# Kernel optimization log

Hardware: AMD Instinct MI355X
Metric: run time of the kernel (lower is better)

The kernel has to match this reference:

```python
import jax, jax.numpy as jnp
import numpy as np

N_NODES = 50000
N_EDGES = 1600000
F_GO, F_RE, F_ME = 512, 256, 256
E_DIM, N_HEADS, H_DIM, O_DIM = 256, 4, 256, 128


def setup_inputs() -> dict:
    key = jax.random.key(0)
    ks = jax.random.split(key, 20)
    s = lambda k, shp, sc: jax.random.normal(k, shp, dtype=jnp.float32) * sc
    inp = {
        "x": jax.random.normal(ks[0], (N_NODES, F_GO + F_RE + F_ME + 1), dtype=jnp.float32),
        "edge_index": jax.random.randint(ks[1], (2, N_EDGES), 0, N_NODES, dtype=jnp.int32),
        # modality projections (stored as [in, out] so we do x @ W)
        "w_go": s(ks[2], (F_GO, E_DIM), 0.04), "b_go": jnp.zeros((E_DIM,), jnp.float32),
        "w_re": s(ks[3], (F_RE, E_DIM), 0.06), "b_re": jnp.zeros((E_DIM,), jnp.float32),
        "w_me": s(ks[4], (F_ME, E_DIM), 0.06), "b_me": jnp.zeros((E_DIM,), jnp.float32),
        "w_gw": s(ks[5], (1, E_DIM), 0.5),    "b_gw": jnp.zeros((E_DIM,), jnp.float32),
        # MultiheadAttention params (torch layout: in_proj_w [3E, E], out_proj_w [E, E])
        "in_proj_w": s(ks[6], (3 * E_DIM, E_DIM), 0.06),
        "in_proj_b": jnp.zeros((3 * E_DIM,), jnp.float32),
        "out_proj_w": s(ks[7], (E_DIM, E_DIM), 0.06),
        "out_proj_b": jnp.zeros((E_DIM,), jnp.float32),
        # GCN layers (stored as [in, out])
        "w1": s(ks[8], (E_DIM, H_DIM), 0.06), "b1": jnp.zeros((H_DIM,), jnp.float32),
        "w2": s(ks[9], (H_DIM, O_DIM), 0.06), "b2": jnp.zeros((O_DIM,), jnp.float32),
    }
    return inp


def _forward(x, edge_index, w_go, b_go, w_re, b_re, w_me, b_me, w_gw, b_gw,
             in_proj_w, in_proj_b, out_proj_w, out_proj_b, w1, b1, w2, b2):
    N = x.shape[0]
    relu = jax.nn.relu
    go = x[:, :F_GO]
    re_ = x[:, F_GO:F_GO + F_RE]
    me = x[:, F_GO + F_RE:F_GO + F_RE + F_ME]
    gw = x[:, -1:]  # gwas = last column
    # [N, 4, E]: four projected modalities stacked as a tiny sequence
    p = jnp.stack([relu(go @ w_go + b_go), relu(re_ @ w_re + b_re),
                   relu(me @ w_me + b_me), relu(gw @ w_gw + b_gw)], axis=1)
    # Multihead self-attention over the 4 modality tokens
    wq, wk, wv = jnp.split(in_proj_w, 3, axis=0)
    bq, bk, bv = jnp.split(in_proj_b, 3, axis=0)
    dh = E_DIM // N_HEADS
    q = (p @ wq.T + bq).reshape(N, 4, N_HEADS, dh)
    k = (p @ wk.T + bk).reshape(N, 4, N_HEADS, dh)
    v = (p @ wv.T + bv).reshape(N, 4, N_HEADS, dh)
    scores = jnp.einsum('nqhd,nkhd->nhqk', q, k) / jnp.sqrt(jnp.float32(dh))
    attn = jax.nn.softmax(scores, axis=-1)
    o = jnp.einsum('nhqk,nkhd->nqhd', attn, v).reshape(N, 4, E_DIM)
    o = o @ out_proj_w.T + out_proj_b
    fused = o.mean(axis=1)  # [N, E]
    # GCN normalization with self-loops (shared by both layers)
    loops = jnp.arange(N, dtype=edge_index.dtype)
    src = jnp.concatenate([edge_index[0], loops])
    dst = jnp.concatenate([edge_index[1], loops])
    deg = jax.ops.segment_sum(jnp.ones_like(src, dtype=fused.dtype), dst, num_segments=N)
    dinv = jnp.where(deg > 0, jax.lax.rsqrt(deg), 0.0)
    norm = dinv[src] * dinv[dst]  # [E+N]

    def gcn(h, W, b):
        hw = h @ W  # transform then scatter-aggregate
        msg = norm[:, None] * hw[src]
        return jax.ops.segment_sum(msg, dst, num_segments=N) + b

    h1 = relu(gcn(fused, w1, b1))
    # dropout p=0.3 skipped (eval mode)
    return gcn(h1, w2, b2)


def reference(x, edge_index, w_go, b_go, w_re, b_re, w_me, b_me, w_gw, b_gw,
              in_proj_w, in_proj_b, out_proj_w, out_proj_b, w1, b1, w2, b2):
    return _forward(x, edge_index, w_go, b_go, w_re, b_re, w_me, b_me, w_gw, b_gw,
                    in_proj_w, in_proj_b, out_proj_w, out_proj_b, w1, b1, w2, b2)
```

## Files before the change

kernel.cpp:

```cpp
#include <hip/hip_runtime.h>
#include <cstdint>
#include <cstddef>

#define NN 50000
#define NE 1600000
#define XD 1025

typedef unsigned short ushortt;
typedef __attribute__((ext_vector_type(8))) short short8;
typedef __attribute__((ext_vector_type(4))) float f32x4;

__device__ __forceinline__ float relu_f(float v) { return v > 0.f ? v : 0.f; }
__device__ __forceinline__ float b2f(ushortt u) { return __uint_as_float(((unsigned)u) << 16); }
__device__ __forceinline__ float blo(unsigned u) { return __uint_as_float(u << 16); }
__device__ __forceinline__ float bhi(unsigned u) { return __uint_as_float(u & 0xffff0000u); }
__device__ __forceinline__ ushortt bf16rn(float f) {
    unsigned u = __float_as_uint(f);
    return (ushortt)((u + 0x7fffu + ((u >> 16) & 1u)) >> 16);
}
__device__ __forceinline__ void load_lds16(const void* g, void* l) {
    __builtin_amdgcn_global_load_lds(
        (const __attribute__((address_space(1))) void*)g,
        (__attribute__((address_space(3))) void*)l, 16, 0, 0);
}

template <int ACT>
__global__ __launch_bounds__(256) void gemm_mfma(
    const ushortt* __restrict__ A, int lda,
    const ushortt* __restrict__ Bt,
    ushortt* __restrict__ C, int ldc,
    const float* __restrict__ bias,
    int M, int K)
{
    __shared__ ushortt As[128 * 32];
    __shared__ ushortt Bs[128 * 32];
    const int tid = threadIdx.x;
    const int w = tid >> 6, l = tid & 63;
    const int wr = w >> 1, wc = w & 1;
    const int brow = blockIdx.y << 7;
    const int bcol = blockIdx.x << 7;

    f32x4 acc[4][4] = {};

    const int rA0 = wr * 64 + (l & 15);
    const int rB0 = wc * 64 + (l & 15);
    const int kslot = l >> 4;

    for (int k0 = 0; k0 < K; k0 += 32) {
#pragma unroll
        for (int c = 0; c < 2; ++c) {
            int rl = c * 64 + w * 16 + (l >> 2);
            int csel = (l & 3) ^ (rl & 3);
            int gr = brow + rl; if (gr >= M) gr = M - 1;
            load_lds16(A + (size_t)gr * lda + k0 + csel * 8, &As[(c * 64 + w * 16) * 32]);
        }
#pragma unroll
        for (int c = 0; c < 2; ++c) {
            int rl = c * 64 + w * 16 + (l >> 2);
            int csel = (l & 3) ^ (rl & 3);
            load_lds16(Bt + (size_t)(bcol + rl) * K + k0 + csel * 8, &Bs[(c * 64 + w * 16) * 32]);
        }
        __syncthreads();

        short8 af[4], bf[4];
#pragma unroll
        for (int mi = 0; mi < 4; ++mi) {
            int row = rA0 + mi * 16;
            af[mi] = *(const short8*)&As[row * 32 + ((kslot ^ (row & 3)) << 3)];
        }
#pragma unroll
        for (int ni = 0; ni < 4; ++ni) {
            int row = rB0 + ni * 16;
            bf[ni] = *(const short8*)&Bs[row * 32 + ((kslot ^ (row & 3)) << 3)];
        }
#pragma unroll
        for (int mi = 0; mi < 4; ++mi)
#pragma unroll
            for (int ni = 0; ni < 4; ++ni)
                acc[mi][ni] = __builtin_amdgcn_mfma_f32_16x16x32_bf16(af[mi], bf[ni], acc[mi][ni], 0, 0, 0);
        __syncthreads();
    }

    const int cb = bcol + wc * 64 + (l & 15);
    const int rb = brow + wr * 64 + ((l >> 4) << 2);
#pragma unroll
    for (int mi = 0; mi < 4; ++mi) {
#pragma unroll
        for (int ni = 0; ni < 4; ++ni) {
            int col = cb + ni * 16;
            float bv = bias ? bias[col] : 0.f;
#pragma unroll
            for (int r = 0; r < 4; ++r) {
                int row = rb + mi * 16 + r;
                if (row < M) {
                    float v = acc[mi][ni][r] + bv;
                    if (ACT == 1) v = relu_f(v);
                    C[(size_t)row * ldc + col] = bf16rn(v);
                }
            }
        }
    }
}

__global__ __launch_bounds__(256) void gemm_branches(
    const ushortt* __restrict__ ago, const ushortt* __restrict__ are, const ushortt* __restrict__ ame,
    const ushortt* __restrict__ wgo, const ushortt* __restrict__ wre, const ushortt* __restrict__ wme,
    const float* __restrict__ b_go, const float* __restrict__ b_re, const float* __restrict__ b_me,
    ushortt* __restrict__ p)
{
    const ushortt* A; const ushortt* Bt; const float* bias; int K, lda, coff;
    if (blockIdx.z == 0)      { A = ago; Bt = wgo; bias = b_go; K = 512; lda = 512; coff = 0; }
    else if (blockIdx.z == 1) { A = are; Bt = wre; bias = b_re; K = 256; lda = 256; coff = 256; }
    else                      { A = ame; Bt = wme; bias = b_me; K = 256; lda = 256; coff = 512; }

    __shared__ ushortt As[128 * 32];
    __shared__ ushortt Bs[128 * 32];
    const int tid = threadIdx.x;
    const int w = tid >> 6, l = tid & 63;
    const int wr = w >> 1, wc = w & 1;
    const int brow = blockIdx.y << 7;
    const int bcol = blockIdx.x << 7;

    f32x4 acc[4][4] = {};

    const int rA0 = wr * 64 + (l & 15);
    const int rB0 = wc * 64 + (l & 15);
    const int kslot = l >> 4;

    for (int k0 = 0; k0 < K; k0 += 32) {
#pragma unroll
        for (int c = 0; c < 2; ++c) {
            int rl = c * 64 + w * 16 + (l >> 2);
            int csel = (l & 3) ^ (rl & 3);
            int gr = brow + rl; if (gr >= NN) gr = NN - 1;
            load_lds16(A + (size_t)gr * lda + k0 + csel * 8, &As[(c * 64 + w * 16) * 32]);
        }
#pragma unroll
        for (int c = 0; c < 2; ++c) {
            int rl = c * 64 + w * 16 + (l >> 2);
            int csel = (l & 3) ^ (rl & 3);
            load_lds16(Bt + (size_t)(bcol + rl) * K + k0 + csel * 8, &Bs[(c * 64 + w * 16) * 32]);
        }
        __syncthreads();

        short8 af[4], bf[4];
#pragma unroll
        for (int mi = 0; mi < 4; ++mi) {
            int row = rA0 + mi * 16;
            af[mi] = *(const short8*)&As[row * 32 + ((kslot ^ (row & 3)) << 3)];
        }
#pragma unroll
        for (int ni = 0; ni < 4; ++ni) {
            int row = rB0 + ni * 16;
            bf[ni] = *(const short8*)&Bs[row * 32 + ((kslot ^ (row & 3)) << 3)];
        }
#pragma unroll
        for (int mi = 0; mi < 4; ++mi)
#pragma unroll
            for (int ni = 0; ni < 4; ++ni)
                acc[mi][ni] = __builtin_amdgcn_mfma_f32_16x16x32_bf16(af[mi], bf[ni], acc[mi][ni], 0, 0, 0);
        __syncthreads();
    }

    const int cb = bcol + wc * 64 + (l & 15);
    const int rb = brow + wr * 64 + ((l >> 4) << 2);
#pragma unroll
    for (int mi = 0; mi < 4; ++mi) {
#pragma unroll
        for (int ni = 0; ni < 4; ++ni) {
            int col = cb + ni * 16;
            float bv = bias[col];
#pragma unroll
            for (int r = 0; r < 4; ++r) {
                int row = rb + mi * 16 + r;
                if (row < NN)
                    p[(size_t)row * 1024 + coff + col] = bf16rn(relu_f(acc[mi][ni][r] + bv));
            }
        }
    }
}

__global__ __launch_bounds__(256) void fused_attn_v7(
    const ushortt* __restrict__ p,
    const ushortt* __restrict__ ipw_opt,
    const float* __restrict__ ipb,
    ushortt* __restrict__ pbar)
{
    __shared__ __align__(16) ushortt p_s[32 * 256];
    __shared__ float asum_s[8][4][4];

    const int tid = threadIdx.x;
    const int w = tid >> 6, l = tid & 63;
    const int nb = blockIdx.x << 3;
    const size_t r0 = (size_t)nb * 4;

    {
        const int slot = l & 31;
#pragma unroll
        for (int c = 0; c < 4; ++c) {
            int row = w * 8 + c * 2 + (l >> 5);
            load_lds16(p + (r0 + row) * 256 + ((slot ^ (row & 7)) << 3),
                       &p_s[(w * 8 + c * 2) * 256]);
        }
    }
    __syncthreads();

    const int nq = w << 6;
    f32x4 aq[2][4] = {}, ak[2][4] = {};
    const int ar0 = l & 15, ar1 = ar0 + 16;
#pragma unroll
    for (int kk = 0; kk < 8; ++kk) {
        const int slot = (kk << 2) + (l >> 4);
        short8 a0 = *(const short8*)&p_s[ar0 * 256 + ((slot ^ (ar0 & 7)) << 3)];
        short8 a1 = *(const short8*)&p_s[ar1 * 256 + ((slot ^ (ar1 & 7)) << 3)];
        short8 bq[4], bk[4];
#pragma unroll
        for (int ni = 0; ni < 4; ++ni) {
            const size_t base = ((((size_t)(w * 8 + kk)) * 4 + ni) * 2) * 512 + (size_t)l * 8;
            bq[ni] = *(const short8*)&ipw_opt[base];
            bk[ni] = *(const short8*)&ipw_opt[base + 512];
        }
#pragma unroll
        for (int ni = 0; ni < 4; ++ni) {
            aq[0][ni] = __builtin_amdgcn_mfma_f32_16x16x32_bf16(a0, bq[ni], aq[0][ni], 0, 0, 0);
            aq[1][ni] = __builtin_amdgcn_mfma_f32_16x16x32_bf16(a1, bq[ni], aq[1][ni], 0, 0, 0);
            ak[0][ni] = __builtin_amdgcn_mfma_f32_16x16x32_bf16(a0, bk[ni], ak[0][ni], 0, 0, 0);
            ak[1][ni] = __builtin_amdgcn_mfma_f32_16x16x32_bf16(a1, bk[ni], ak[1][ni], 0, 0, 0);
        }
    }

    float bqv[4], bkv[4];
#pragma unroll
    for (int ni = 0; ni < 4; ++ni) {
        int col = nq + (ni << 4) + (l & 15);
        bqv[ni] = ipb[col];
        bkv[ni] = ipb[256 + col];
    }
#pragma unroll
    for (int mt = 0; mt < 2; ++mt) {
        float s[4][4] = {};
#pragma unroll
        for (int ni = 0; ni < 4; ++ni) {
            float qv[4], kv[4];
#pragma unroll
            for (int r = 0; r < 4; ++r) {
                qv[r] = aq[mt][ni][r] + bqv[ni];
                kv[r] = ak[mt][ni][r] + bkv[ni];
            }
#pragma unroll
            for (int ti = 0; ti < 4; ++ti)
#pragma unroll
                for (int tj = 0; tj < 4; ++tj)
                    s[ti][tj] = fmaf(qv[ti], kv[tj], s[ti][tj]);
        }
#pragma unroll
        for (int m = 1; m <= 8; m <<= 1)
#pragma unroll
            for (int ti = 0; ti < 4; ++ti)
#pragma unroll
                for (int tj = 0; tj < 4; ++tj)
                    s[ti][tj] += __shfl_xor(s[ti][tj], m);
        float asum[4] = {};
#pragma unroll
        for (int ti = 0; ti < 4; ++ti) {
            float v0 = s[ti][0] * 0.125f, v1 = s[ti][1] * 0.125f;
            float v2 = s[ti][2] * 0.125f, v3 = s[ti][3] * 0.125f;
            float m4 = fmaxf(fmaxf(v0, v1), fmaxf(v2, v3));
            float e0 = __expf(v0 - m4), e1 = __expf(v1 - m4);
            float e2 = __expf(v2 - m4), e3 = __expf(v3 - m4);
            float inv = 1.f / (e0 + e1 + e2 + e3);
            asum[0] = fmaf(e0, inv, asum[0]);
            asum[1] = fmaf(e1, inv, asum[1]);
            asum[2] = fmaf(e2, inv, asum[2]);
            asum[3] = fmaf(e3, inv, asum[3]);
        }
        if ((l & 15) == 0) {
            int node = mt * 4 + (l >> 4);
#pragma unroll
            for (int tj = 0; tj < 4; ++tj)
                asum_s[node][w][tj] = 0.25f * asum[tj];
        }
    }
    __syncthreads();

    {
        const int node = tid >> 5;
        const int c8 = (tid & 31) << 3;
        float f[4][8];
#pragma unroll
        for (int tj = 0; tj < 4; ++tj) {
            int row = node * 4 + tj;
            uint4 u = *(const uint4*)&p_s[row * 256 + (((c8 >> 3) ^ (row & 7)) << 3)];
            f[tj][0] = blo(u.x); f[tj][1] = bhi(u.x); f[tj][2] = blo(u.y); f[tj][3] = bhi(u.y);
            f[tj][4] = blo(u.z); f[tj][5] = bhi(u.z); f[tj][6] = blo(u.w); f[tj][7] = bhi(u.w);
        }
#pragma unroll
        for (int h = 0; h < 4; ++h) {
            float a0 = asum_s[node][h][0], a1 = asum_s[node][h][1];
            float a2 = asum_s[node][h][2], a3 = asum_s[node][h][3];
            ushortt res[8];
#pragma unroll
            for (int i = 0; i < 8; ++i)
                res[i] = bf16rn(a0 * f[0][i] + a1 * f[1][i] + a2 * f[2][i] + a3 * f[3][i]);
            *(uint4*)&pbar[(size_t)(nb + node) * 1024 + h * 256 + c8] = *(uint4*)res;
        }
    }
}

__global__ __launch_bounds__(256) void prep_T(
    const float* __restrict__ opw, const float* __restrict__ w1, float* __restrict__ T)
{
    int d = blockIdx.x, c = threadIdx.x;
    float a = 0.f;
    for (int j = 0; j < 256; ++j)
        a = fmaf(opw[j * 256 + d], w1[j * 256 + c], a);
    T[d * 256 + c] = a;
}

__global__ __launch_bounds__(256) void prep_wbig(
    const float* __restrict__ wv, const float* __restrict__ T, ushortt* __restrict__ wbigT)
{
    int c = blockIdx.x, kk = threadIdx.x;
#pragma unroll
    for (int h = 0; h < 4; ++h) {
        float a = 0.f;
        for (int d = 0; d < 64; ++d)
            a = fmaf(wv[(h * 64 + d) * 256 + kk], T[(h * 64 + d) * 256 + c], a);
        wbigT[(size_t)c * 1024 + h * 256 + kk] = bf16rn(a);
    }
}

__global__ __launch_bounds__(256) void prep_bbig(
    const float* __restrict__ opb, const float* __restrict__ w1,
    const float* __restrict__ ipb, const float* __restrict__ T,
    float* __restrict__ bbig)
{
    int c = threadIdx.x;
    float a = 0.f;
    for (int j = 0; j < 256; ++j) a = fmaf(opb[j], w1[j * 256 + c], a);
    for (int d = 0; d < 256; ++d) a = fmaf(ipb[512 + d], T[d * 256 + c], a);
    bbig[c] = a;
}

__global__ __launch_bounds__(256) void conv_all(
    const float* __restrict__ w_go, const float* __restrict__ w_re,
    const float* __restrict__ w_me, const float* __restrict__ w2,
    const float* __restrict__ ipw,
    ushortt* __restrict__ o_go, ushortt* __restrict__ o_re,
    ushortt* __restrict__ o_me, ushortt* __restrict__ o_w2,
    ushortt* __restrict__ o_ip)
{
    int idx = blockIdx.x * 256 + threadIdx.x;
    if (idx < 131072) {
        int c = idx >> 9, r = idx & 511;
        o_go[idx] = bf16rn(w_go[r * 256 + c]);
    } else if (idx < 196608) {
        int j = idx - 131072; int c = j >> 8, r = j & 255;
        o_re[j] = bf16rn(w_re[r * 256 + c]);
    } else if (idx < 262144) {
        int j = idx - 196608; int c = j >> 8, r = j & 255;
        o_me[j] = bf16rn(w_me[r * 256 + c]);
    } else if (idx < 294912) {
        int j = idx - 262144; int c = j >> 8, r = j & 255;
        o_w2[j] = bf16rn(w2[r * 128 + c]);
    } else if (idx < 425984) {
        int j5 = idx - 294912;
        int j  = j5 & 7;
        int l  = (j5 >> 3) & 63;
        int qk = (j5 >> 9) & 1;
        int ni = (j5 >> 10) & 3;
        int kk = (j5 >> 12) & 7;
        int w  = (j5 >> 15) & 3;
        int row = qk * 256 + w * 64 + ni * 16 + (l & 15);
        int col = kk * 32 + ((l >> 4) << 3) + j;
        o_ip[j5] = bf16rn(ipw[(size_t)row * 256 + col]);
    }
}

__global__ __launch_bounds__(256) void conv_x(
    const float* __restrict__ x, ushortt* __restrict__ ago,
    ushortt* __restrict__ are, ushortt* __restrict__ ame)
{
    long idx = blockIdx.x * 256L + threadIdx.x;
    if (idx >= (long)NN * 128) return;
    int n = (int)(idx >> 7);
    int c8 = ((int)idx & 127) << 3;
    const float* src = x + (size_t)n * XD + c8;
    ushortt* dst;
    if (c8 < 512) dst = ago + (size_t)n * 512 + c8;
    else if (c8 < 768) dst = are + (size_t)n * 256 + (c8 - 512);
    else dst = ame + (size_t)n * 256 + (c8 - 768);
    ushort4 o1, o2;
    o1.x = bf16rn(src[0]); o1.y = bf16rn(src[1]); o1.z = bf16rn(src[2]); o1.w = bf16rn(src[3]);
    o2.x = bf16rn(src[4]); o2.y = bf16rn(src[5]); o2.z = bf16rn(src[6]); o2.w = bf16rn(src[7]);
    *(ushort4*)dst = o1;
    *(ushort4*)(dst + 4) = o2;
}

__global__ __launch_bounds__(256) void gw_kernel(
    const float* __restrict__ x, const float* __restrict__ w_gw,
    const float* __restrict__ b_gw, ushortt* __restrict__ p)
{
    long idx = blockIdx.x * 256L + threadIdx.x;
    if (idx >= (long)NN * 64) return;
    int n = (int)(idx >> 6);
    int c = ((int)idx & 63) << 2;
    float g = x[(size_t)n * XD + 1024];
    float4 w4 = *(const float4*)(w_gw + c);
    float4 b4 = *(const float4*)(b_gw + c);
    ushort4 r;
    r.x = bf16rn(relu_f(fmaf(g, w4.x, b4.x)));
    r.y = bf16rn(relu_f(fmaf(g, w4.y, b4.y)));
    r.z = bf16rn(relu_f(fmaf(g, w4.z, b4.z)));
    r.w = bf16rn(relu_f(fmaf(g, w4.w, b4.w)));
    *(ushort4*)(p + (size_t)n * 1024 + 768 + c) = r;
}

__global__ __launch_bounds__(256) void deg_int_kernel(
    const int* __restrict__ dst, int* __restrict__ deg, int E)
{
    int e = (blockIdx.x * 256 + threadIdx.x) * 4;
    if (e >= E) return;
    int4 d = *(const int4*)(dst + e);
    atomicAdd(&deg[d.x], 1);
    atomicAdd(&deg[d.y], 1);
    atomicAdd(&deg[d.z], 1);
    atomicAdd(&deg[d.w], 1);
}

__global__ __launch_bounds__(256) void dinv_kernel(
    const int* __restrict__ deg, float* __restrict__ dinv, int N)
{
    int n = blockIdx.x * 256 + threadIdx.x;
    if (n < N) dinv[n] = rsqrtf((float)deg[n] + 1.0f);
}

__global__ __launch_bounds__(1024) void scan_blk(
    const int* __restrict__ deg, int* __restrict__ offs, int* __restrict__ btot, int N)
{
    __shared__ int wsum[16];
    const int tid = threadIdx.x;
    const int lane = tid & 63;
    const int w = tid >> 6;
    int i = blockIdx.x * 1024 + tid;
    int v = (i < N) ? deg[i] : 0;
    int x = v;
#pragma unroll
    for (int d = 1; d < 64; d <<= 1) {
        int t = __shfl_up(x, d);
        if (lane >= d) x += t;
    }
    if (lane == 63) wsum[w] = x;
    __syncthreads();
    if (w == 0 && lane < 16) {
        int y = wsum[lane];
#pragma unroll
        for (int d = 1; d < 16; d <<= 1) {
            int t = __shfl_up(y, d);
            if (lane >= d) y += t;
        }
        wsum[lane] = y;
    }
    __syncthreads();
    int waveoff = (w == 0) ? 0 : wsum[w - 1];
    if (i < N) offs[i] = waveoff + x - v;
    if (tid == 0) btot[blockIdx.x] = wsum[15];
}

__global__ __launch_bounds__(64) void scan_tot(int* __restrict__ btot, int nb)
{
    int t = threadIdx.x;
    int v = (t < nb) ? btot[t] : 0;
    int x = v;
#pragma unroll
    for (int d = 1; d < 64; d <<= 1) {
        int tt = __shfl_up(x, d);
        if (t >= d) x += tt;
    }
    if (t < nb) btot[t] = x - v;
    if (t == 63) btot[nb] = x;
}

__global__ __launch_bounds__(256) void scan_add(
    const int* __restrict__ btot, int* __restrict__ offs, int N, int nb)
{
    int i = blockIdx.x * 256 + threadIdx.x;
    if (i < N) offs[i] += btot[i >> 10];
    else if (i == N) offs[N] = btot[nb];
}

__global__ __launch_bounds__(256) void csr_fill(
    const int* __restrict__ ei, const int* __restrict__ offs,
    int* __restrict__ cursor, int2* __restrict__ pk,
    const float* __restrict__ dinv, int E)
{
    for (int e = blockIdx.x * 256 + threadIdx.x; e < E; e += gridDim.x * 256) {
        int s = ei[e];
        int d = ei[NE + e];
        int pos = offs[d] + atomicAdd(&cursor[d], 1);
        pk[pos] = make_int2(s, __float_as_int(dinv[s] * dinv[d]));
    }
}

template <int ACT, int OUTBF>
__global__ __launch_bounds__(256) void gcn_gather256(
    const int* __restrict__ offs, const int2* __restrict__ pk,
    const ushortt* __restrict__ hw,
    const float* __restrict__ dinv, const float* __restrict__ bias,
    void* __restrict__ outb, int N)
{
    __shared__ float part[2][256];
    const int tid = threadIdx.x;
    const int nodei = tid >> 7;
    const int half = (tid >> 6) & 1;
    const int l = tid & 63;
    const int wid = blockIdx.x * 2 + nodei;
    const int col = l * 4;
    const bool active = wid < N;

    int beg = 0, end = 0;
    if (active) { beg = offs[wid]; end = offs[wid + 1]; }
    const int mid = beg + ((end - beg + 1) >> 1);
    int e = half ? mid : beg;
    const int ee = half ? end : mid;

    float acc[4] = {0.f, 0.f, 0.f, 0.f};
    if (active && half == 0) {
        float self = dinv[wid] * dinv[wid];
        ushort4 r = *(const ushort4*)(hw + (size_t)wid * 256 + col);
        acc[0] = self * b2f(r.x); acc[1] = self * b2f(r.y);
        acc[2] = self * b2f(r.z); acc[3] = self * b2f(r.w);
    }

    for (; e + 7 < ee; e += 8) {
        int2 q[8];
#pragma unroll
        for (int j = 0; j < 8; ++j) q[j] = pk[e + j];
        ushort4 r[8];
#pragma unroll
        for (int j = 0; j < 8; ++j) r[j] = *(const ushort4*)(hw + (size_t)q[j].x * 256 + col);
#pragma unroll
        for (int j = 0; j < 8; ++j) {
            float n = __int_as_float(q[j].y);
            acc[0] = fmaf(n, b2f(r[j].x), acc[0]); acc[1] = fmaf(n, b2f(r[j].y), acc[1]);
            acc[2] = fmaf(n, b2f(r[j].z), acc[2]); acc[3] = fmaf(n, b2f(r[j].w), acc[3]);
        }
    }
    for (; e < ee; ++e) {
        int2 p0 = pk[e];
        float n0 = __int_as_float(p0.y);
        ushort4 r0 = *(const ushort4*)(hw + (size_t)p0.x * 256 + col);
        acc[0] = fmaf(n0, b2f(r0.x), acc[0]); acc[1] = fmaf(n0, b2f(r0.y), acc[1]);
        acc[2] = fmaf(n0, b2f(r0.z), acc[2]); acc[3] = fmaf(n0, b2f(r0.w), acc[3]);
    }

    if (half == 1) {
        float4 v; v.x = acc[0]; v.y = acc[1]; v.z = acc[2]; v.w = acc[3];
        *(float4*)&part[nodei][col] = v;
    }
    __syncthreads();
    if (active && half == 0) {
        float4 pv = *(const float4*)&part[nodei][col];
        acc[0] += pv.x; acc[1] += pv.y; acc[2] += pv.z; acc[3] += pv.w;
#pragma unroll
        for (int jj = 0; jj < 4; ++jj) {
            acc[jj] += bias[col + jj];
            if (ACT == 1) acc[jj] = relu_f(acc[jj]);
        }
        if (OUTBF == 1) {
            ushortt* ob = (ushortt*)outb;
            ushort4 r;
            r.x = bf16rn(acc[0]); r.y = bf16rn(acc[1]); r.z = bf16rn(acc[2]); r.w = bf16rn(acc[3]);
            *(ushort4*)(ob + (size_t)wid * 256 + col) = r;
        } else {
            float* ob = (float*)outb;
            float4 r; r.x = acc[0]; r.y = acc[1]; r.z = acc[2]; r.w = acc[3];
            *(float4*)(ob + (size_t)wid * 256 + col) = r;
        }
    }
}

__global__ __launch_bounds__(256) void gcn_gather128(
    const int* __restrict__ offs, const int2* __restrict__ pk,
    const ushortt* __restrict__ hw,
    const float* __restrict__ dinv, const float* __restrict__ bias,
    float* __restrict__ outb, int N)
{
    const int wid = blockIdx.x * 4 + (threadIdx.x >> 6);
    const int lane = threadIdx.x & 63;
    if (wid >= N) return;
    const int g = lane >> 5;
    const int col = (lane & 31) * 4;

    float acc[4] = {0.f, 0.f, 0.f, 0.f};
    if (g == 0) {
        float self = dinv[wid] * dinv[wid];
        ushort4 r = *(const ushort4*)(hw + (size_t)wid * 128 + col);
        acc[0] = self * b2f(r.x); acc[1] = self * b2f(r.y);
        acc[2] = self * b2f(r.z); acc[3] = self * b2f(r.w);
    }

    const int beg = offs[wid], end = offs[wid + 1];
    int e = beg + g;
    for (; e + 6 < end; e += 8) {
        int2 q[4];
        q[0] = pk[e]; q[1] = pk[e + 2]; q[2] = pk[e + 4]; q[3] = pk[e + 6];
        ushort4 r[4];
#pragma unroll
        for (int j = 0; j < 4; ++j) r[j] = *(const ushort4*)(hw + (size_t)q[j].x * 128 + col);
#pragma unroll
        for (int j = 0; j < 4; ++j) {
            float n = __int_as_float(q[j].y);
            acc[0] = fmaf(n, b2f(r[j].x), acc[0]); acc[1] = fmaf(n, b2f(r[j].y), acc[1]);
            acc[2] = fmaf(n, b2f(r[j].z), acc[2]); acc[3] = fmaf(n, b2f(r[j].w), acc[3]);
        }
    }
    for (; e < end; e += 2) {
        int2 p0 = pk[e];
        float n0 = __int_as_float(p0.y);
        ushort4 r0 = *(const ushort4*)(hw + (size_t)p0.x * 128 + col);
        acc[0] = fmaf(n0, b2f(r0.x), acc[0]); acc[1] = fmaf(n0, b2f(r0.y), acc[1]);
        acc[2] = fmaf(n0, b2f(r0.z), acc[2]); acc[3] = fmaf(n0, b2f(r0.w), acc[3]);
    }

#pragma unroll
    for (int jj = 0; jj < 4; ++jj)
        acc[jj] += __shfl_xor(acc[jj], 32);

    if (g == 0) {
        float4 r;
        r.x = acc[0] + bias[col + 0];
        r.y = acc[1] + bias[col + 1];
        r.z = acc[2] + bias[col + 2];
        r.w = acc[3] + bias[col + 3];
        *(float4*)(outb + (size_t)wid * 128 + col) = r;
    }
}

extern "C" void kernel_launch(void* const* d_in, const int* in_sizes, int n_in,
                              void* d_out, int out_size, void* d_ws, size_t ws_size,
                              hipStream_t stream)
{
    const float* x    = (const float*)d_in[0];
    const int*   ei   = (const int*)d_in[1];
    const float* w_go = (const float*)d_in[2];
    const float* b_go = (const float*)d_in[3];
    const float* w_re = (const float*)d_in[4];
    const float* b_re = (const float*)d_in[5];
    const float* w_me = (const float*)d_in[6];
    const float* b_me = (const float*)d_in[7];
    const float* w_gw = (const float*)d_in[8];
    const float* b_gw = (const float*)d_in[9];
    const float* ipw  = (const float*)d_in[10];
    const float* ipb  = (const float*)d_in[11];
    const float* opw  = (const float*)d_in[12];
    const float* opb  = (const float*)d_in[13];
    const float* w1   = (const float*)d_in[14];
    const float* b1   = (const float*)d_in[15];
    const float* w2   = (const float*)d_in[16];
    const float* b2   = (const float*)d_in[17];
    float* out = (float*)d_out;
    char* ws   = (char*)d_ws;

    size_t off = 0;
    auto alloc = [&](size_t bytes) { size_t o = off; off += (bytes + 255) & ~(size_t)255; return o; };
    const size_t o_dinv = alloc(NN * 4);
    const size_t o_deg  = alloc(NN * 4);
    const size_t o_offs = alloc((NN + 1) * 4);
    const size_t o_cur  = alloc(NN * 4);
    const size_t o_btot = alloc(64 * 4);
    const size_t o_csrp = alloc((size_t)NE * 8);
    const size_t o_wgo  = alloc(256 * 512 * 2);
    const size_t o_wre  = alloc(256 * 256 * 2);
    const size_t o_wme  = alloc(256 * 256 * 2);
    const size_t o_ipw  = alloc(512 * 256 * 2);
    const size_t o_T    = alloc(256 * 256 * 4);
    const size_t o_wbig = alloc(256 * 1024 * 2);
    const size_t o_bbig = alloc(256 * 4);
    const size_t o_w2t  = alloc(128 * 256 * 2);
    const size_t o_pbr  = alloc((size_t)4 * NN * 256 * 2);
    const size_t o_x16  = alloc((size_t)NN * 1024 * 2);
    const size_t o_pbar = alloc((size_t)NN * 1024 * 2);
    const size_t o_hw   = alloc((size_t)NN * 256 * 2);
    const size_t o_h1   = alloc((size_t)NN * 256 * 2);
    const size_t o_hw2  = alloc((size_t)NN * 128 * 2);

    float* f_dinv = (float*)(ws + o_dinv);
    int*   i_deg  = (int*)(ws + o_deg);
    int*   i_offs = (int*)(ws + o_offs);
    int*   i_cur  = (int*)(ws + o_cur);
    int*   i_btot = (int*)(ws + o_btot);
    int2*  i_csrp = (int2*)(ws + o_csrp);
    float* f_T    = (float*)(ws + o_T);
    float* f_bbig = (float*)(ws + o_bbig);
    ushortt* p    = (ushortt*)(ws + o_pbr);
    ushortt* ago  = (ushortt*)(ws + o_x16);
    ushortt* are  = ago + (size_t)NN * 512;
    ushortt* ame  = ago + (size_t)NN * 768;
    ushortt* pbar = (ushortt*)(ws + o_pbar);
    ushortt* hw   = (ushortt*)(ws + o_hw);
    ushortt* h1   = (ushortt*)(ws + o_h1);
    ushortt* hw2  = (ushortt*)(ws + o_hw2);

    const int NB_SCAN = (NN + 1023) / 1024;

    hipMemsetAsync(i_deg, 0, NN * 4, stream);
    hipMemsetAsync(i_cur, 0, NN * 4, stream);
    deg_int_kernel<<<(NE / 4 + 255) / 256, 256, 0, stream>>>(ei + NE, i_deg, NE);
    dinv_kernel<<<(NN + 255) / 256, 256, 0, stream>>>(i_deg, f_dinv, NN);
    scan_blk<<<NB_SCAN, 1024, 0, stream>>>(i_deg, i_offs, i_btot, NN);
    scan_tot<<<1, 64, 0, stream>>>(i_btot, NB_SCAN);
    scan_add<<<(NN + 1 + 255) / 256, 256, 0, stream>>>(i_btot, i_offs, NN, NB_SCAN);
    csr_fill<<<1024, 256, 0, stream>>>(ei, i_offs, i_cur, i_csrp, f_dinv, NE);

    conv_all<<<(425984 + 255) / 256, 256, 0, stream>>>(
        w_go, w_re, w_me, w2, ipw,
        (ushortt*)(ws + o_wgo), (ushortt*)(ws + o_wre), (ushortt*)(ws + o_wme),
        (ushortt*)(ws + o_w2t), (ushortt*)(ws + o_ipw));
    prep_T<<<256, 256, 0, stream>>>(opw, w1, f_T);
    prep_wbig<<<256, 256, 0, stream>>>(ipw + 512 * 256, f_T, (ushortt*)(ws + o_wbig));
    prep_bbig<<<1, 256, 0, stream>>>(opb, w1, ipb, f_T, f_bbig);

    conv_x<<<((long)NN * 128 + 255) / 256, 256, 0, stream>>>(x, ago, are, ame);

    dim3 gBr(2, (NN + 127) / 128, 3);
    gemm_branches<<<gBr, 256, 0, stream>>>(
        ago, are, ame,
        (ushortt*)(ws + o_wgo), (ushortt*)(ws + o_wre), (ushortt*)(ws + o_wme),
        b_go, b_re, b_me, p);
    gw_kernel<<<((long)NN * 64 + 255) / 256, 256, 0, stream>>>(x, w_gw, b_gw, p);

    fused_attn_v7<<<NN / 8, 256, 0, stream>>>(p, (ushortt*)(ws + o_ipw), ipb, pbar);

    dim3 gB(2, (NN + 127) / 128);
    gemm_mfma<0><<<gB, 256, 0, stream>>>(pbar, 1024, (ushortt*)(ws + o_wbig), hw, 256, f_bbig, NN, 1024);

    gcn_gather256<1, 1><<<(NN + 1) / 2, 256, 0, stream>>>(i_offs, i_csrp, hw, f_dinv, b1, h1, NN);

    dim3 gH2(1, (NN + 127) / 128);
    gemm_mfma<0><<<gH2, 256, 0, stream>>>(h1, 256, (ushortt*)(ws + o_w2t), hw2, 128, nullptr, NN, 256);
    gcn_gather128<<<(NN + 3) / 4, 256, 0, stream>>>(i_offs, i_csrp, hw2, f_dinv, b2, out, NN);
}
```

Measured before the change: 760.8 us.

## Merge independent prep, conversion, CSR-fill and branch GEMM kernels into mega-kernels

Several independent launches are merged into three block-range-dispatched kernels: x conversion, degree counting, weight conversion, gwas projection and T prep in one; wbig, bbig and dinv in another; CSR fill together with the branch GEMMs in a third. This removes launch gaps and lets the latency-bound atomic CSR fill overlap with MFMA GEMM work. The cost is heterogeneous blocks sharing one launch, so the LDS allocation and register pressure of the GEMM path apply to the CSR-fill blocks too.

```diff
diff --git a/kernel.cpp b/kernel.cpp
--- a/kernel.cpp
+++ b/kernel.cpp
@@ -102,24 +102,212 @@
     }
 }
 
-__global__ __launch_bounds__(256) void gemm_branches(
+__global__ __launch_bounds__(256) void mega_a(
+    const float* __restrict__ x, const int* __restrict__ dst, int* __restrict__ deg,
+    const float* __restrict__ w_go, const float* __restrict__ w_re,
+    const float* __restrict__ w_me, const float* __restrict__ w2,
+    const float* __restrict__ ipw,
+    ushortt* __restrict__ o_go, ushortt* __restrict__ o_re,
+    ushortt* __restrict__ o_me, ushortt* __restrict__ o_w2, ushortt* __restrict__ o_ip,
+    ushortt* __restrict__ ago, ushortt* __restrict__ are, ushortt* __restrict__ ame,
+    const float* __restrict__ w_gw, const float* __restrict__ b_gw, ushortt* __restrict__ p,
+    const float* __restrict__ opw, const float* __restrict__ w1, float* __restrict__ T)
+{
+    const int bid = blockIdx.x;
+    const int tid = threadIdx.x;
+    if (bid < 25000) {
+        long idx = bid * 256L + tid;
+        int n = (int)(idx >> 7);
+        int c8 = ((int)idx & 127) << 3;
+        const float* src = x + (size_t)n * XD + c8;
+        ushortt* dstp;
+        if (c8 < 512) dstp = ago + (size_t)n * 512 + c8;
+        else if (c8 < 768) dstp = are + (size_t)n * 256 + (c8 - 512);
+        else dstp = ame + (size_t)n * 256 + (c8 - 768);
+        ushort4 o1, o2;
+        o1.x = bf16rn(src[0]); o1.y = bf16rn(src[1]); o1.z = bf16rn(src[2]); o1.w = bf16rn(src[3]);
+        o2.x = bf16rn(src[4]); o2.y = bf16rn(src[5]); o2.z = bf16rn(src[6]); o2.w = bf16rn(src[7]);
+        *(ushort4*)dstp = o1;
+        *(ushort4*)(dstp + 4) = o2;
+    } else if (bid < 26563) {
+        int e = ((bid - 25000) * 256 + tid) * 4;
+        if (e < NE) {
+            int4 d = *(const int4*)(dst + e);
+            atomicAdd(&deg[d.x], 1);
+            atomicAdd(&deg[d.y], 1);
+            atomicAdd(&deg[d.z], 1);
+            atomicAdd(&deg[d.w], 1);
+        }
+    } else if (bid < 28227) {
+        int idx = (bid - 26563) * 256 + tid;
+        if (idx < 131072) {
+            int c = idx >> 9, r = idx & 511;
+            o_go[idx] = bf16rn(w_go[r * 256 + c]);
+        } else if (idx < 196608) {
+            int j = idx - 131072; int c = j >> 8, r = j & 255;
+            o_re[j] = bf16rn(w_re[r * 256 + c]);
+        } else if (idx < 262144) {
+            int j = idx - 196608; int c = j >> 8, r = j & 255;
+            o_me[j] = bf16rn(w_me[r * 256 + c]);
+        } else if (idx < 294912) {
+            int j = idx - 262144; int c = j >> 8, r = j & 255;
+            o_w2[j] = bf16rn(w2[r * 128 + c]);
+        } else {
+            int j5 = idx - 294912;
+            int j  = j5 & 7;
+            int l  = (j5 >> 3) & 63;
+            int qk = (j5 >> 9) & 1;
+            int ni = (j5 >> 10) & 3;
+            int kk = (j5 >> 12) & 7;
+            int w  = (j5 >> 15) & 3;
+            int row = qk * 256 + w * 64 + ni * 16 + (l & 15);
+            int col = kk * 32 + ((l >> 4) << 3) + j;
+            o_ip[j5] = bf16rn(ipw[(size_t)row * 256 + col]);
+        }
+    } else if (bid < 40727) {
+        long idx = (bid - 28227) * 256L + tid;
+        int n = (int)(idx >> 6);
+        int c = ((int)idx & 63) << 2;
+        float g = x[(size_t)n * XD + 1024];
+        float4 w4 = *(const float4*)(w_gw + c);
+        float4 b4 = *(const float4*)(b_gw + c);
+        ushort4 r;
+        r.x = bf16rn(relu_f(fmaf(g, w4.x, b4.x)));
+        r.y = bf16rn(relu_f(fmaf(g, w4.y, b4.y)));
+        r.z = bf16rn(relu_f(fmaf(g, w4.z, b4.z)));
+        r.w = bf16rn(relu_f(fmaf(g, w4.w, b4.w)));
+        *(ushort4*)(p + (size_t)n * 1024 + 768 + c) = r;
+    } else {
+        int d = bid - 40727, c = tid;
+        float a = 0.f;
+        for (int j = 0; j < 256; ++j)
+            a = fmaf(opw[j * 256 + d], w1[j * 256 + c], a);
+        T[d * 256 + c] = a;
+    }
+}
+
+__global__ __launch_bounds__(256) void mega_c(
+    const float* __restrict__ ipw, const float* __restrict__ T, ushortt* __restrict__ wbigT,
+    const float* __restrict__ opb, const float* __restrict__ w1,
+    const float* __restrict__ ipb, float* __restrict__ bbig,
+    const int* __restrict__ deg, float* __restrict__ dinv)
+{
+    const int bid = blockIdx.x;
+    const int tid = threadIdx.x;
+    if (bid < 256) {
+        const float* wv = ipw + 512 * 256;
+        int c = bid, kk = tid;
+#pragma unroll
+        for (int h = 0; h < 4; ++h) {
+            float a = 0.f;
+            for (int d = 0; d < 64; ++d)
+                a = fmaf(wv[(h * 64 + d) * 256 + kk], T[(h * 64 + d) * 256 + c], a);
+            wbigT[(size_t)c * 1024 + h * 256 + kk] = bf16rn(a);
+        }
+    } else if (bid == 256) {
+        int c = tid;
+        float a = 0.f;
+        for (int j = 0; j < 256; ++j) a = fmaf(opb[j], w1[j * 256 + c], a);
+        for (int d = 0; d < 256; ++d) a = fmaf(ipb[512 + d], T[d * 256 + c], a);
+        bbig[c] = a;
+    } else {
+        int n = (bid - 257) * 256 + tid;
+        if (n < NN) dinv[n] = rsqrtf((float)deg[n] + 1.0f);
+    }
+}
+
+__global__ __launch_bounds__(1024) void scan_blk(
+    const int* __restrict__ deg, int* __restrict__ offs, int* __restrict__ btot, int N)
+{
+    __shared__ int wsum[16];
+    const int tid = threadIdx.x;
+    const int lane = tid & 63;
+    const int w = tid >> 6;
+    int i = blockIdx.x * 1024 + tid;
+    int v = (i < N) ? deg[i] : 0;
+    int x = v;
+#pragma unroll
+    for (int d = 1; d < 64; d <<= 1) {
+        int t = __shfl_up(x, d);
+        if (lane >= d) x += t;
+    }
+    if (lane == 63) wsum[w] = x;
+    __syncthreads();
+    if (w == 0 && lane < 16) {
+        int y = wsum[lane];
+#pragma unroll
+        for (int d = 1; d < 16; d <<= 1) {
+            int t = __shfl_up(y, d);
+            if (lane >= d) y += t;
+        }
+        wsum[lane] = y;
+    }
+    __syncthreads();
+    int waveoff = (w == 0) ? 0 : wsum[w - 1];
+    if (i < N) offs[i] = waveoff + x - v;
+    if (tid == 0) btot[blockIdx.x] = wsum[15];
+}
+
+__global__ __launch_bounds__(64) void scan_tot(int* __restrict__ btot, int nb)
+{
+    int t = threadIdx.x;
+    int v = (t < nb) ? btot[t] : 0;
+    int x = v;
+#pragma unroll
+    for (int d = 1; d < 64; d <<= 1) {
+        int tt = __shfl_up(x, d);
+        if (t >= d) x += tt;
+    }
+    if (t < nb) btot[t] = x - v;
+    if (t == 63) btot[nb] = x;
+}
+
+__global__ __launch_bounds__(256) void scan_add(
+    const int* __restrict__ btot, int* __restrict__ offs, int N, int nb)
+{
+    int i = blockIdx.x * 256 + threadIdx.x;
+    if (i < N) offs[i] += btot[i >> 10];
+    else if (i == N) offs[N] = btot[nb];
+}
+
+__global__ __launch_bounds__(256) void mega_b(
+    const int* __restrict__ ei, const int* __restrict__ offs,
+    int* __restrict__ cursor, int2* __restrict__ pk, const float* __restrict__ dinv,
     const ushortt* __restrict__ ago, const ushortt* __restrict__ are, const ushortt* __restrict__ ame,
     const ushortt* __restrict__ wgo, const ushortt* __restrict__ wre, const ushortt* __restrict__ wme,
     const float* __restrict__ b_go, const float* __restrict__ b_re, const float* __restrict__ b_me,
     ushortt* __restrict__ p)
 {
-    const ushortt* A; const ushortt* Bt; const float* bias; int K, lda, coff;
-    if (blockIdx.z == 0)      { A = ago; Bt = wgo; bias = b_go; K = 512; lda = 512; coff = 0; }
-    else if (blockIdx.z == 1) { A = are; Bt = wre; bias = b_re; K = 256; lda = 256; coff = 256; }
-    else                      { A = ame; Bt = wme; bias = b_me; K = 256; lda = 256; coff = 512; }
-
     __shared__ ushortt As[128 * 32];
     __shared__ ushortt Bs[128 * 32];
+    const int bid = blockIdx.x;
     const int tid = threadIdx.x;
+
+    if (bid < 1024) {
+        for (int e = bid * 256 + tid; e < NE; e += 1024 * 256) {
+            int s = ei[e];
+            int d = ei[NE + e];
+            int pos = offs[d] + atomicAdd(&cursor[d], 1);
+            pk[pos] = make_int2(s, __float_as_int(dinv[s] * dinv[d]));
+        }
+        return;
+    }
+
+    const int t = bid - 1024;
+    const int z = t / 782;
+    const int r = t - z * 782;
+    const int by = r >> 1;
+    const int bx = r & 1;
+
+    const ushortt* A; const ushortt* Bt; const float* bias; int K, lda, coff;
+    if (z == 0)      { A = ago; Bt = wgo; bias = b_go; K = 512; lda = 512; coff = 0; }
+    else if (z == 1) { A = are; Bt = wre; bias = b_re; K = 256; lda = 256; coff = 256; }
+    else             { A = ame; Bt = wme; bias = b_me; K = 256; lda = 256; coff = 512; }
+
     const int w = tid >> 6, l = tid & 63;
     const int wr = w >> 1, wc = w & 1;
-    const int brow = blockIdx.y << 7;
-    const int bcol = blockIdx.x << 7;
+    const int brow = by << 7;
+    const int bcol = bx << 7;
 
     f32x4 acc[4][4] = {};
 
@@ -171,10 +359,10 @@
             int col = cb + ni * 16;
             float bv = bias[col];
 #pragma unroll
-            for (int r = 0; r < 4; ++r) {
-                int row = rb + mi * 16 + r;
+            for (int rr = 0; rr < 4; ++rr) {
+                int row = rb + mi * 16 + rr;
                 if (row < NN)
-                    p[(size_t)row * 1024 + coff + col] = bf16rn(relu_f(acc[mi][ni][r] + bv));
+                    p[(size_t)row * 1024 + coff + col] = bf16rn(relu_f(acc[mi][ni][rr] + bv));
             }
         }
     }
@@ -304,201 +492,6 @@
                 res[i] = bf16rn(a0 * f[0][i] + a1 * f[1][i] + a2 * f[2][i] + a3 * f[3][i]);
             *(uint4*)&pbar[(size_t)(nb + node) * 1024 + h * 256 + c8] = *(uint4*)res;
         }
-    }
-}
-
-__global__ __launch_bounds__(256) void prep_T(
-    const float* __restrict__ opw, const float* __restrict__ w1, float* __restrict__ T)
-{
-    int d = blockIdx.x, c = threadIdx.x;
-    float a = 0.f;
-    for (int j = 0; j < 256; ++j)
-        a = fmaf(opw[j * 256 + d], w1[j * 256 + c], a);
-    T[d * 256 + c] = a;
-}
-
-__global__ __launch_bounds__(256) void prep_wbig(
-    const float* __restrict__ wv, const float* __restrict__ T, ushortt* __restrict__ wbigT)
-{
-    int c = blockIdx.x, kk = threadIdx.x;
-#pragma unroll
-    for (int h = 0; h < 4; ++h) {
-        float a = 0.f;
-        for (int d = 0; d < 64; ++d)
-            a = fmaf(wv[(h * 64 + d) * 256 + kk], T[(h * 64 + d) * 256 + c], a);
-        wbigT[(size_t)c * 1024 + h * 256 + kk] = bf16rn(a);
-    }
-}
-
-__global__ __launch_bounds__(256) void prep_bbig(
-    const float* __restrict__ opb, const float* __restrict__ w1,
-    const float* __restrict__ ipb, const float* __restrict__ T,
-    float* __restrict__ bbig)
-{
-    int c = threadIdx.x;
-    float a = 0.f;
-    for (int j = 0; j < 256; ++j) a = fmaf(opb[j], w1[j * 256 + c], a);
-    for (int d = 0; d < 256; ++d) a = fmaf(ipb[512 + d], T[d * 256 + c], a);
-    bbig[c] = a;
-}
-
-__global__ __launch_bounds__(256) void conv_all(
-    const float* __restrict__ w_go, const float* __restrict__ w_re,
-    const float* __restrict__ w_me, const float* __restrict__ w2,
-    const float* __restrict__ ipw,
-    ushortt* __restrict__ o_go, ushortt* __restrict__ o_re,
-    ushortt* __restrict__ o_me, ushortt* __restrict__ o_w2,
-    ushortt* __restrict__ o_ip)
-{
-    int idx = blockIdx.x * 256 + threadIdx.x;
-    if (idx < 131072) {
-        int c = idx >> 9, r = idx & 511;
-        o_go[idx] = bf16rn(w_go[r * 256 + c]);
-    } else if (idx < 196608) {
-        int j = idx - 131072; int c = j >> 8, r = j & 255;
-        o_re[j] = bf16rn(w_re[r * 256 + c]);
-    } else if (idx < 262144) {
-        int j = idx - 196608; int c = j >> 8, r = j & 255;
-        o_me[j] = bf16rn(w_me[r * 256 + c]);
-    } else if (idx < 294912) {
-        int j = idx - 262144; int c = j >> 8, r = j & 255;
-        o_w2[j] = bf16rn(w2[r * 128 + c]);
-    } else if (idx < 425984) {
-        int j5 = idx - 294912;
-        int j  = j5 & 7;
-        int l  = (j5 >> 3) & 63;
-        int qk = (j5 >> 9) & 1;
-        int ni = (j5 >> 10) & 3;
-        int kk = (j5 >> 12) & 7;
-        int w  = (j5 >> 15) & 3;
-        int row = qk * 256 + w * 64 + ni * 16 + (l & 15);
-        int col = kk * 32 + ((l >> 4) << 3) + j;
-        o_ip[j5] = bf16rn(ipw[(size_t)row * 256 + col]);
-    }
-}
-
-__global__ __launch_bounds__(256) void conv_x(
-    const float* __restrict__ x, ushortt* __restrict__ ago,
-    ushortt* __restrict__ are, ushortt* __restrict__ ame)
-{
-    long idx = blockIdx.x * 256L + threadIdx.x;
-    if (idx >= (long)NN * 128) return;
-    int n = (int)(idx >> 7);
-    int c8 = ((int)idx & 127) << 3;
-    const float* src = x + (size_t)n * XD + c8;
-    ushortt* dst;
-    if (c8 < 512) dst = ago + (size_t)n * 512 + c8;
-    else if (c8 < 768) dst = are + (size_t)n * 256 + (c8 - 512);
-    else dst = ame + (size_t)n * 256 + (c8 - 768);
-    ushort4 o1, o2;
-    o1.x = bf16rn(src[0]); o1.y = bf16rn(src[1]); o1.z = bf16rn(src[2]); o1.w = bf16rn(src[3]);
-    o2.x = bf16rn(src[4]); o2.y = bf16rn(src[5]); o2.z = bf16rn(src[6]); o2.w = bf16rn(src[7]);
-    *(ushort4*)dst = o1;
-    *(ushort4*)(dst + 4) = o2;
-}
-
-__global__ __launch_bounds__(256) void gw_kernel(
-    const float* __restrict__ x, const float* __restrict__ w_gw,
-    const float* __restrict__ b_gw, ushortt* __restrict__ p)
-{
-    long idx = blockIdx.x * 256L + threadIdx.x;
-    if (idx >= (long)NN * 64) return;
-    int n = (int)(idx >> 6);
-    int c = ((int)idx & 63) << 2;
-    float g = x[(size_t)n * XD + 1024];
-    float4 w4 = *(const float4*)(w_gw + c);
-    float4 b4 = *(const float4*)(b_gw + c);
-    ushort4 r;
-    r.x = bf16rn(relu_f(fmaf(g, w4.x, b4.x)));
-    r.y = bf16rn(relu_f(fmaf(g, w4.y, b4.y)));
-    r.z = bf16rn(relu_f(fmaf(g, w4.z, b4.z)));
-    r.w = bf16rn(relu_f(fmaf(g, w4.w, b4.w)));
-    *(ushort4*)(p + (size_t)n * 1024 + 768 + c) = r;
-}
-
-__global__ __launch_bounds__(256) void deg_int_kernel(
-    const int* __restrict__ dst, int* __restrict__ deg, int E)
-{
-    int e = (blockIdx.x * 256 + threadIdx.x) * 4;
-    if (e >= E) return;
-    int4 d = *(const int4*)(dst + e);
-    atomicAdd(&deg[d.x], 1);
-    atomicAdd(&deg[d.y], 1);
-    atomicAdd(&deg[d.z], 1);
-    atomicAdd(&deg[d.w], 1);
-}
-
-__global__ __launch_bounds__(256) void dinv_kernel(
-    const int* __restrict__ deg, float* __restrict__ dinv, int N)
-{
-    int n = blockIdx.x * 256 + threadIdx.x;
-    if (n < N) dinv[n] = rsqrtf((float)deg[n] + 1.0f);
-}
-
-__global__ __launch_bounds__(1024) void scan_blk(
-    const int* __restrict__ deg, int* __restrict__ offs, int* __restrict__ btot, int N)
-{
-    __shared__ int wsum[16];
-    const int tid = threadIdx.x;
-    const int lane = tid & 63;
-    const int w = tid >> 6;
-    int i = blockIdx.x * 1024 + tid;
-    int v = (i < N) ? deg[i] : 0;
-    int x = v;
-#pragma unroll
-    for (int d = 1; d < 64; d <<= 1) {
-        int t = __shfl_up(x, d);
-        if (lane >= d) x += t;
-    }
-    if (lane == 63) wsum[w] = x;
-    __syncthreads();
-    if (w == 0 && lane < 16) {
-        int y = wsum[lane];
-#pragma unroll
-        for (int d = 1; d < 16; d <<= 1) {
-            int t = __shfl_up(y, d);
-            if (lane >= d) y += t;
-        }
-        wsum[lane] = y;
-    }
-    __syncthreads();
-    int waveoff = (w == 0) ? 0 : wsum[w - 1];
-    if (i < N) offs[i] = waveoff + x - v;
-    if (tid == 0) btot[blockIdx.x] = wsum[15];
-}
-
-__global__ __launch_bounds__(64) void scan_tot(int* __restrict__ btot, int nb)
-{
-    int t = threadIdx.x;
-    int v = (t < nb) ? btot[t] : 0;
-    int x = v;
-#pragma unroll
-    for (int d = 1; d < 64; d <<= 1) {
-        int tt = __shfl_up(x, d);
-        if (t >= d) x += tt;
-    }
-    if (t < nb) btot[t] = x - v;
-    if (t == 63) btot[nb] = x;
-}
-
-__global__ __launch_bounds__(256) void scan_add(
-    const int* __restrict__ btot, int* __restrict__ offs, int N, int nb)
-{
-    int i = blockIdx.x * 256 + threadIdx.x;
-    if (i < N) offs[i] += btot[i >> 10];
-    else if (i == N) offs[N] = btot[nb];
-}
-
-__global__ __launch_bounds__(256) void csr_fill(
-    const int* __restrict__ ei, const int* __restrict__ offs,
-    int* __restrict__ cursor, int2* __restrict__ pk,
-    const float* __restrict__ dinv, int E)
-{
-    for (int e = blockIdx.x * 256 + threadIdx.x; e < E; e += gridDim.x * 256) {
-        int s = ei[e];
-        int d = ei[NE + e];
-        int pos = offs[d] + atomicAdd(&cursor[d], 1);
-        pk[pos] = make_int2(s, __float_as_int(dinv[s] * dinv[d]));
     }
 }
 
@@ -706,29 +699,30 @@
 
     hipMemsetAsync(i_deg, 0, NN * 4, stream);
     hipMemsetAsync(i_cur, 0, NN * 4, stream);
-    deg_int_kernel<<<(NE / 4 + 255) / 256, 256, 0, stream>>>(ei + NE, i_deg, NE);
-    dinv_kernel<<<(NN + 255) / 256, 256, 0, stream>>>(i_deg, f_dinv, NN);
+
+    mega_a<<<40983, 256, 0, stream>>>(
+        x, ei + NE, i_deg,
+        w_go, w_re, w_me, w2, ipw,
+        (ushortt*)(ws + o_wgo), (ushortt*)(ws + o_wre), (ushortt*)(ws + o_wme),
+        (ushortt*)(ws + o_w2t), (ushortt*)(ws + o_ipw),
+        ago, are, ame,
+        w_gw, b_gw, p,
+        opw, w1, f_T);
+
+    mega_c<<<453, 256, 0, stream>>>(
+        ipw, f_T, (ushortt*)(ws + o_wbig),
+        opb, w1, ipb, f_bbig,
+        i_deg, f_dinv);
+
     scan_blk<<<NB_SCAN, 1024, 0, stream>>>(i_deg, i_offs, i_btot, NN);
     scan_tot<<<1, 64, 0, stream>>>(i_btot, NB_SCAN);
     scan_add<<<(NN + 1 + 255) / 256, 256, 0, stream>>>(i_btot, i_offs, NN, NB_SCAN);
-    csr_fill<<<1024, 256, 0, stream>>>(ei, i_offs, i_cur, i_csrp, f_dinv, NE);
-
-    conv_all<<<(425984 + 255) / 256, 256, 0, stream>>>(
-        w_go, w_re, w_me, w2, ipw,
-        (ushortt*)(ws + o_wgo), (ushortt*)(ws + o_wre), (ushortt*)(ws + o_wme),
-        (ushortt*)(ws + o_w2t), (ushortt*)(ws + o_ipw));
-    prep_T<<<256, 256, 0, stream>>>(opw, w1, f_T);
-    prep_wbig<<<256, 256, 0, stream>>>(ipw + 512 * 256, f_T, (ushortt*)(ws + o_wbig));
-    prep_bbig<<<1, 256, 0, stream>>>(opb, w1, ipb, f_T, f_bbig);
-
-    conv_x<<<((long)NN * 128 + 255) / 256, 256, 0, stream>>>(x, ago, are, ame);
-
-    dim3 gBr(2, (NN + 127) / 128, 3);
-    gemm_branches<<<gBr, 256, 0, stream>>>(
+
+    mega_b<<<1024 + 2346, 256, 0, stream>>>(
+        ei, i_offs, i_cur, i_csrp, f_dinv,
         ago, are, ame,
         (ushortt*)(ws + o_wgo), (ushortt*)(ws + o_wre), (ushortt*)(ws + o_wme),
         b_go, b_re, b_me, p);
-    gw_kernel<<<((long)NN * 64 + 255) / 256, 256, 0, stream>>>(x, w_gw, b_gw, p);
 
     fused_attn_v7<<<NN / 8, 256, 0, stream>>>(p, (ushortt*)(ws + o_ipw), ipb, pbar);
 
```

Measured after the change: 704.3 us. -7.4%, faster.
